# Performance work log

Hardware: AMD Instinct MI355X
Metric: run time of the kernel (lower is better)

The kernel has to match this reference:

```python
import jax, jax.numpy as jnp
import numpy as np

FEATURES = 768

def setup_inputs() -> dict:
    key = jax.random.key(0)
    k1, k2, kq, kd, kc = jax.random.split(key, 5)
    B, S1, S2 = 8, 2048, 2048
    bound = 1.0 / np.sqrt(FEATURES)  # nn.Linear default init range
    return {
        "matrix1": jax.random.normal(k1, (B, S1, FEATURES), dtype=jnp.float32),
        "matrix2": jax.random.normal(k2, (B, S2, FEATURES), dtype=jnp.float32),
        "w_q": jax.random.uniform(kq, (FEATURES,), jnp.float32, -bound, bound),
        "w_d": jax.random.uniform(kd, (FEATURES,), jnp.float32, -bound, bound),
        "w_c": jax.random.uniform(kc, (FEATURES,), jnp.float32, -bound, bound),
    }

def reference(matrix1, matrix2, w_q, w_d, w_c):
    # S[b,j,k] = (m1 @ w_q)[b,j] + (m2 @ w_d)[b,k] + sum_f w_c[f]*m1[b,j,f]*m2[b,k,f]
    Q = jnp.einsum('bjf,f->bj', matrix1, w_q)                # [B, S1]
    D = jnp.einsum('bkf,f->bk', matrix2, w_d)                # [B, S2]
    C = jnp.einsum('bjf,bkf->bjk', matrix1 * w_c, matrix2)   # [B, S1, S2]
    return Q[:, :, None] + D[:, None, :] + C
```

## Files before the change

### kernel.cpp

```cpp
#include <hip/hip_runtime.h>
#include <hip/hip_bf16.h>

#define S1 2048
#define S2 2048
#define FEAT 768
#define NB 8
#define BM 256
#define BN 256
#define BK 32
#define NKT (FEAT / BK)
#define KTILE_BYTES 32768
#define NBUF 4

typedef __attribute__((ext_vector_type(8))) short bf16x8;
typedef __attribute__((ext_vector_type(4))) float f32x4;
typedef __attribute__((ext_vector_type(4))) unsigned short us4;
typedef __attribute__((address_space(1))) const unsigned int gu32;
typedef __attribute__((address_space(3))) unsigned int lu32;

static __device__ __forceinline__ unsigned short f2bf(float x) {
    unsigned u = __builtin_bit_cast(unsigned, x);
    unsigned r = u + 0x7FFFu + ((u >> 16) & 1u);
    return (unsigned short)(r >> 16);
}

__global__ __launch_bounds__(256) void conv_kernel(
    const float* __restrict__ m1, const float* __restrict__ m2,
    const float* __restrict__ wq, const float* __restrict__ wd,
    const float* __restrict__ wc,
    unsigned short* __restrict__ A, unsigned short* __restrict__ Bm,
    float* __restrict__ Q, float* __restrict__ D) {
    int wave = threadIdx.x >> 6;
    int lane = threadIdx.x & 63;
    int g = blockIdx.x * 4 + wave;
    bool isA = (g < NB * S1);
    int row = isA ? g : g - NB * S1;
    const float* src = isA ? m1 : m2;
    const float* w   = isA ? wq : wd;
    unsigned short* dst = (isA ? A : Bm) + (size_t)row * FEAT;
    const float4* rp = (const float4*)(src + (size_t)row * FEAT);
    const float4* wp = (const float4*)w;
    const float4* cp = (const float4*)wc;
    float acc = 0.f;
#pragma unroll
    for (int i = 0; i < 3; ++i) {
        int idx = lane + 64 * i;
        float4 a = rp[idx];
        float4 b = wp[idx];
        acc += a.x * b.x + a.y * b.y + a.z * b.z + a.w * b.w;
        float4 c;
        if (isA) c = cp[idx]; else c = float4{1.f, 1.f, 1.f, 1.f};
        us4 v = { f2bf(a.x * c.x), f2bf(a.y * c.y),
                  f2bf(a.z * c.z), f2bf(a.w * c.w) };
        *(us4*)(dst + idx * 4) = v;
    }
#pragma unroll
    for (int s = 32; s; s >>= 1) acc += __shfl_xor(acc, s, 64);
    if (lane == 0) (isA ? Q : D)[row] = acc;
}

#define STAGE(kt) do {                                                            \
    const int _buf = (kt) & (NBUF - 1);                                           \
    const char* _As = Ab + (kt) * (BK * 2);                                       \
    const char* _Bs = Bb + (kt) * (BK * 2);                                       \
    char* _lA = ldsb + _buf * KTILE_BYTES;                                        \
    char* _lB = _lA + 16384;                                                      \
    _Pragma("unroll")                                                             \
    for (int _r = 0; _r < 2; ++_r) {                                              \
        const int _rowb = _r * 128 + wave * 16;                                   \
        __builtin_amdgcn_global_load_lds(                                         \
            (gu32*)(_As + (size_t)(_rowb + srow) * (FEAT * 2) + scolsw),          \
            (lu32*)(_lA + _rowb * 64), 16, 0, 0);                                 \
        __builtin_amdgcn_global_load_lds(                                         \
            (gu32*)(_Bs + (size_t)(_rowb + srow) * (FEAT * 2) + scolsw),          \
            (lu32*)(_lB + _rowb * 64), 16, 0, 0);                                 \
    }                                                                             \
} while (0)

#define LOADFRAGS(set, ktidx) do {                                                \
    const char* _lA = ldsb + ((ktidx) & (NBUF - 1)) * KTILE_BYTES;                \
    const char* _lB = _lA + 16384;                                                \
    _Pragma("unroll")                                                             \
    for (int _n = 0; _n < 4; ++_n)                                                \
        bfx[set][_n] = *(const bf16x8*)(_lB + (wn * 64 + _n * 16 + fr) * 64 + fkb);\
    _Pragma("unroll")                                                             \
    for (int _m = 0; _m < 8; ++_m)                                                \
        afr[set][_m] = *(const bf16x8*)(_lA + (wm * 128 + _m * 16 + fr) * 64 + fkb);\
} while (0)

__global__ __launch_bounds__(512, 2) void gemm256_kernel(
    const unsigned short* __restrict__ A, const unsigned short* __restrict__ Bm,
    const float* __restrict__ Q, const float* __restrict__ D,
    float* __restrict__ out) {

    extern __shared__ __align__(16) char ldsb[];

    const int bid = blockIdx.x;
    const int swz = (bid & 7) * 64 + (bid >> 3);
    const int b  = swz >> 6;
    const int t  = swz & 63;
    const int tm = t >> 3, tn = t & 7;

    const int tid  = threadIdx.x;
    const int lane = tid & 63;
    const int wave = tid >> 6;
    const int wm = wave >> 2, wn = wave & 3;

    const char* Ab = (const char*)(A + ((size_t)b * S1 + (size_t)tm * BM) * FEAT);
    const char* Bb = (const char*)(Bm + ((size_t)b * S2 + (size_t)tn * BN) * FEAT);

    const int srow   = lane >> 2;
    const int scolsw = (((lane & 3) ^ ((lane >> 3) & 3)) * 16);

    const int fr  = lane & 15;
    const int fkb = (((lane >> 4) ^ ((lane >> 1) & 3)) * 16);

    f32x4 acc[8][4];
#pragma unroll
    for (int m = 0; m < 8; ++m)
#pragma unroll
        for (int n = 0; n < 4; ++n) acc[m][n] = (f32x4)0.f;

    bf16x8 afr[2][8];
    bf16x8 bfx[2][4];

    STAGE(0);
    STAGE(1);
    STAGE(2);
    asm volatile("s_waitcnt vmcnt(4)" ::: "memory");
    __builtin_amdgcn_s_barrier();
    asm volatile("" ::: "memory");
    LOADFRAGS(0, 0);

#pragma unroll 2
    for (int kt = 0; kt < NKT; ++kt) {
        const int cur = kt & 1, nxt = cur ^ 1;
        if (kt + 3 < NKT) STAGE(kt + 3);
        if (kt + 1 < NKT) LOADFRAGS(nxt, kt + 1);

        __builtin_amdgcn_s_setprio(1);
#pragma unroll
        for (int m = 0; m < 8; ++m)
#pragma unroll
            for (int n = 0; n < 4; ++n)
                acc[m][n] = __builtin_amdgcn_mfma_f32_16x16x32_bf16(
                    afr[cur][m], bfx[cur][n], acc[m][n], 0, 0, 0);
        __builtin_amdgcn_s_setprio(0);

        if (kt + 1 < NKT) {
            if (kt + 3 < NKT) asm volatile("s_waitcnt vmcnt(4)" ::: "memory");
            else              asm volatile("s_waitcnt vmcnt(0)" ::: "memory");
            __builtin_amdgcn_s_barrier();
            asm volatile("" ::: "memory");
        }
    }

    const float* Qb = Q + b * S1 + tm * BM;
    const float* Db = D + b * S2 + tn * BN;
    float dv[4];
#pragma unroll
    for (int n = 0; n < 4; ++n) dv[n] = Db[wn * 64 + n * 16 + fr];

    const size_t outbase = ((size_t)b * S1 + (size_t)tm * BM) * S2 + (size_t)tn * BN;
#pragma unroll
    for (int m = 0; m < 8; ++m) {
#pragma unroll
        for (int i = 0; i < 4; ++i) {
            int rl = wm * 128 + m * 16 + (lane >> 4) * 4 + i;
            float qv = Qb[rl];
            float* orow = out + outbase + (size_t)rl * S2 + wn * 64;
#pragma unroll
            for (int n = 0; n < 4; ++n)
                orow[n * 16 + fr] = acc[m][n][i] + qv + dv[n];
        }
    }
}

__global__ __launch_bounds__(256) void qd_kernel(
    const float* __restrict__ m1, const float* __restrict__ m2,
    const float* __restrict__ wq, const float* __restrict__ wd,
    float* __restrict__ Q, float* __restrict__ D) {
    int wave = threadIdx.x >> 6;
    int lane = threadIdx.x & 63;
    int g = blockIdx.x * 4 + wave;
    const float* src; const float* w; float* dst; int row;
    if (g < NB * S1) { src = m1; w = wq; dst = Q; row = g; }
    else             { src = m2; w = wd; dst = D; row = g - NB * S1; }
    const float4* rp = (const float4*)(src + (size_t)row * FEAT);
    const float4* wp = (const float4*)w;
    float acc = 0.f;
#pragma unroll
    for (int i = 0; i < 3; ++i) {
        float4 a = rp[lane + 64 * i];
        float4 b = wp[lane + 64 * i];
        acc += a.x * b.x + a.y * b.y + a.z * b.z + a.w * b.w;
    }
#pragma unroll
    for (int s = 32; s; s >>= 1) acc += __shfl_xor(acc, s, 64);
    if (lane == 0) dst[row] = acc;
}

__global__ __launch_bounds__(256) void gemm_kernel(
    const float* __restrict__ m1, const float* __restrict__ m2,
    const float* __restrict__ wc,
    const float* __restrict__ Q, const float* __restrict__ D,
    float* __restrict__ out) {

    __shared__ __align__(16) char sA[128 * 64 * 2];
    __shared__ __align__(16) char sB[128 * 64 * 2];
    __shared__ float wcs[FEAT];

    const int tid = threadIdx.x;
    const int blk = blockIdx.x;
    const int b  = blk >> 8;
    const int t  = blk & 255;
    const int tm = t >> 4, tn = t & 15;

    for (int i = tid; i < FEAT; i += 256) wcs[i] = wc[i];

    const float* Abase = m1 + ((size_t)b * S1 + (size_t)tm * 128) * FEAT;
    const float* Bbase = m2 + ((size_t)b * S2 + (size_t)tn * 128) * FEAT;

    const int lane = tid & 63;
    const int wave = tid >> 6;
    const int wm = wave >> 1, wn = wave & 1;

    f32x4 acc[4][4];
#pragma unroll
    for (int m = 0; m < 4; ++m)
#pragma unroll
        for (int n = 0; n < 4; ++n) acc[m][n] = (f32x4)0.f;

    const int col4 = tid & 15;
    const int row0 = tid >> 4;

    __syncthreads();

    for (int ks = 0; ks < FEAT / 64; ++ks) {
        float4 wc4 = *(const float4*)&wcs[ks * 64 + col4 * 4];
        const float4* Ak = (const float4*)(Abase + ks * 64);
        const float4* Bk = (const float4*)(Bbase + ks * 64);

        __syncthreads();
#pragma unroll
        for (int i = 0; i < 8; ++i) {
            int r = row0 + 16 * i;
            float4 a = Ak[(size_t)r * (FEAT / 4) + col4];
            us4 av = { f2bf(a.x * wc4.x), f2bf(a.y * wc4.y),
                       f2bf(a.z * wc4.z), f2bf(a.w * wc4.w) };
            int off = r * 128 + ((col4 * 8) ^ ((r & 7) << 4));
            *(us4*)(sA + off) = av;
        }
#pragma unroll
        for (int i = 0; i < 8; ++i) {
            int r = row0 + 16 * i;
            float4 v = Bk[(size_t)r * (FEAT / 4) + col4];
            us4 bv = { f2bf(v.x), f2bf(v.y), f2bf(v.z), f2bf(v.w) };
            int off = r * 128 + ((col4 * 8) ^ ((r & 7) << 4));
            *(us4*)(sB + off) = bv;
        }
        __syncthreads();

#pragma unroll
        for (int s = 0; s < 2; ++s) {
            bf16x8 af[4], bfr[4];
#pragma unroll
            for (int m = 0; m < 4; ++m) {
                int r = wm * 64 + m * 16 + (lane & 15);
                int coff = (s * 64 + (lane >> 4) * 16) ^ ((r & 7) << 4);
                af[m] = *(const bf16x8*)(sA + r * 128 + coff);
            }
#pragma unroll
            for (int n = 0; n < 4; ++n) {
                int r = wn * 64 + n * 16 + (lane & 15);
                int coff = (s * 64 + (lane >> 4) * 16) ^ ((r & 7) << 4);
                bfr[n] = *(const bf16x8*)(sB + r * 128 + coff);
            }
#pragma unroll
            for (int m = 0; m < 4; ++m)
#pragma unroll
                for (int n = 0; n < 4; ++n)
                    acc[m][n] = __builtin_amdgcn_mfma_f32_16x16x32_bf16(
                        af[m], bfr[n], acc[m][n], 0, 0, 0);
        }
    }

    const float* Qb = Q + b * S1 + tm * 128;
    const float* Db = D + b * S2 + tn * 128;
    float dv[4];
#pragma unroll
    for (int n = 0; n < 4; ++n) dv[n] = Db[wn * 64 + n * 16 + (lane & 15)];

    const size_t outbase = ((size_t)b * S1 + (size_t)tm * 128) * S2 + (size_t)tn * 128;
#pragma unroll
    for (int m = 0; m < 4; ++m) {
#pragma unroll
        for (int i = 0; i < 4; ++i) {
            int rl = wm * 64 + m * 16 + (lane >> 4) * 4 + i;
            float qv = Qb[rl];
            float* orow = out + outbase + (size_t)rl * S2 + wn * 64;
#pragma unroll
            for (int n = 0; n < 4; ++n) {
                int cl = n * 16 + (lane & 15);
                orow[cl] = acc[m][n][i] + qv + dv[n];
            }
        }
    }
}

extern "C" void kernel_launch(void* const* d_in, const int* in_sizes, int n_in,
                              void* d_out, int out_size, void* d_ws, size_t ws_size,
                              hipStream_t stream) {
    const float* m1 = (const float*)d_in[0];
    const float* m2 = (const float*)d_in[1];
    const float* wq = (const float*)d_in[2];
    const float* wd = (const float*)d_in[3];
    const float* wc = (const float*)d_in[4];
    float* out = (float*)d_out;

    const size_t elems = (size_t)NB * S1 * FEAT;
    const size_t need = 2 * elems * sizeof(unsigned short)
                      + (size_t)(NB * S1 + NB * S2) * sizeof(float);

    if (ws_size >= need) {
        unsigned short* Abuf = (unsigned short*)d_ws;
        unsigned short* Bbuf = Abuf + elems;
        float* Q  = (float*)(Bbuf + elems);
        float* Dv = Q + NB * S1;
        conv_kernel<<<(NB * S1 + NB * S2) / 4, 256, 0, stream>>>(
            m1, m2, wq, wd, wc, Abuf, Bbuf, Q, Dv);
        gemm256_kernel<<<NB * (S1 / BM) * (S2 / BN), 512, NBUF * KTILE_BYTES, stream>>>(
            Abuf, Bbuf, Q, Dv, out);
    } else {
        float* Q  = (float*)d_ws;
        float* Dv = Q + NB * S1;
        qd_kernel<<<(2 * NB * S1) / 4, 256, 0, stream>>>(m1, m2, wq, wd, Q, Dv);
        gemm_kernel<<<NB * 256, 256, 0, stream>>>(m1, m2, wc, Q, Dv, out);
    }
}
```

Before: 93.29 us.

## Split GEMM main loop into two interleaved phases with staged loads and fragment reads

Each k-iteration now runs as two halves. The A and B global-to-LDS loads and the next-fragment LDS reads are spread across two MFMA clusters, with extra barriers between them, to interleave memory traffic with compute more finely (ping-pong style). Launch bounds drop from 2 to 1 blocks per SM, which gives the compiler more registers but may reduce occupancy. The extra barriers add sync cost per iteration.

```diff
diff --git a/kernel.cpp b/kernel.cpp
--- a/kernel.cpp
+++ b/kernel.cpp
@@ -59,36 +59,17 @@
     if (lane == 0) (isA ? Q : D)[row] = acc;
 }
 
-#define STAGE(kt) do {                                                            \
-    const int _buf = (kt) & (NBUF - 1);                                           \
-    const char* _As = Ab + (kt) * (BK * 2);                                       \
-    const char* _Bs = Bb + (kt) * (BK * 2);                                       \
-    char* _lA = ldsb + _buf * KTILE_BYTES;                                        \
-    char* _lB = _lA + 16384;                                                      \
+#define STAGE_HALF(_src, _ldst) do {                                              \
     _Pragma("unroll")                                                             \
     for (int _r = 0; _r < 2; ++_r) {                                              \
         const int _rowb = _r * 128 + wave * 16;                                   \
         __builtin_amdgcn_global_load_lds(                                         \
-            (gu32*)(_As + (size_t)(_rowb + srow) * (FEAT * 2) + scolsw),          \
-            (lu32*)(_lA + _rowb * 64), 16, 0, 0);                                 \
-        __builtin_amdgcn_global_load_lds(                                         \
-            (gu32*)(_Bs + (size_t)(_rowb + srow) * (FEAT * 2) + scolsw),          \
-            (lu32*)(_lB + _rowb * 64), 16, 0, 0);                                 \
+            (gu32*)((_src) + (size_t)(_rowb + srow) * (FEAT * 2) + scolsw),       \
+            (lu32*)((_ldst) + _rowb * 64), 16, 0, 0);                             \
     }                                                                             \
 } while (0)
 
-#define LOADFRAGS(set, ktidx) do {                                                \
-    const char* _lA = ldsb + ((ktidx) & (NBUF - 1)) * KTILE_BYTES;                \
-    const char* _lB = _lA + 16384;                                                \
-    _Pragma("unroll")                                                             \
-    for (int _n = 0; _n < 4; ++_n)                                                \
-        bfx[set][_n] = *(const bf16x8*)(_lB + (wn * 64 + _n * 16 + fr) * 64 + fkb);\
-    _Pragma("unroll")                                                             \
-    for (int _m = 0; _m < 8; ++_m)                                                \
-        afr[set][_m] = *(const bf16x8*)(_lA + (wm * 128 + _m * 16 + fr) * 64 + fkb);\
-} while (0)
-
-__global__ __launch_bounds__(512, 2) void gemm256_kernel(
+__global__ __launch_bounds__(512, 1) void gemm256_kernel(
     const unsigned short* __restrict__ A, const unsigned short* __restrict__ Bm,
     const float* __restrict__ Q, const float* __restrict__ D,
     float* __restrict__ out) {
@@ -124,32 +105,74 @@
     bf16x8 afr[2][8];
     bf16x8 bfx[2][4];
 
-    STAGE(0);
-    STAGE(1);
-    STAGE(2);
+#pragma unroll
+    for (int pk = 0; pk < 3; ++pk) {
+        char* lA = ldsb + pk * KTILE_BYTES;
+        STAGE_HALF(Ab + pk * (BK * 2), lA);
+        STAGE_HALF(Bb + pk * (BK * 2), lA + 16384);
+    }
     asm volatile("s_waitcnt vmcnt(4)" ::: "memory");
     __builtin_amdgcn_s_barrier();
     asm volatile("" ::: "memory");
-    LOADFRAGS(0, 0);
+    {
+        const char* lA = ldsb;
+        const char* lB = ldsb + 16384;
+#pragma unroll
+        for (int n = 0; n < 4; ++n)
+            bfx[0][n] = *(const bf16x8*)(lB + (wn * 64 + n * 16 + fr) * 64 + fkb);
+#pragma unroll
+        for (int m = 0; m < 8; ++m)
+            afr[0][m] = *(const bf16x8*)(lA + (wm * 128 + m * 16 + fr) * 64 + fkb);
+    }
 
 #pragma unroll 2
     for (int kt = 0; kt < NKT; ++kt) {
         const int cur = kt & 1, nxt = cur ^ 1;
-        if (kt + 3 < NKT) STAGE(kt + 3);
-        if (kt + 1 < NKT) LOADFRAGS(nxt, kt + 1);
-
+        const int lk = kt + 3;
+        const char* nA = ldsb + ((kt + 1) & 3) * KTILE_BYTES;
+        const char* nB = nA + 16384;
+        char* stA = ldsb + (lk & 3) * KTILE_BYTES;
+
+        if (lk < NKT) STAGE_HALF(Ab + lk * (BK * 2), stA);
+        if (kt + 1 < NKT) {
+#pragma unroll
+            for (int n = 0; n < 4; ++n)
+                bfx[nxt][n] = *(const bf16x8*)(nB + (wn * 64 + n * 16 + fr) * 64 + fkb);
+#pragma unroll
+            for (int m = 0; m < 2; ++m)
+                afr[nxt][m] = *(const bf16x8*)(nA + (wm * 128 + m * 16 + fr) * 64 + fkb);
+        }
+        __builtin_amdgcn_s_barrier();
+        asm volatile("" ::: "memory");
         __builtin_amdgcn_s_setprio(1);
 #pragma unroll
-        for (int m = 0; m < 8; ++m)
+        for (int m = 0; m < 4; ++m)
 #pragma unroll
             for (int n = 0; n < 4; ++n)
                 acc[m][n] = __builtin_amdgcn_mfma_f32_16x16x32_bf16(
                     afr[cur][m], bfx[cur][n], acc[m][n], 0, 0, 0);
         __builtin_amdgcn_s_setprio(0);
 
+        if (lk < NKT) STAGE_HALF(Bb + lk * (BK * 2), stA + 16384);
         if (kt + 1 < NKT) {
-            if (kt + 3 < NKT) asm volatile("s_waitcnt vmcnt(4)" ::: "memory");
-            else              asm volatile("s_waitcnt vmcnt(0)" ::: "memory");
+#pragma unroll
+            for (int m = 2; m < 8; ++m)
+                afr[nxt][m] = *(const bf16x8*)(nA + (wm * 128 + m * 16 + fr) * 64 + fkb);
+        }
+        __builtin_amdgcn_s_barrier();
+        asm volatile("" ::: "memory");
+        __builtin_amdgcn_s_setprio(1);
+#pragma unroll
+        for (int m = 4; m < 8; ++m)
+#pragma unroll
+            for (int n = 0; n < 4; ++n)
+                acc[m][n] = __builtin_amdgcn_mfma_f32_16x16x32_bf16(
+                    afr[cur][m], bfx[cur][n], acc[m][n], 0, 0, 0);
+        __builtin_amdgcn_s_setprio(0);
+
+        if (kt + 1 < NKT) {
+            if (lk < NKT) asm volatile("s_waitcnt vmcnt(4)" ::: "memory");
+            else          asm volatile("s_waitcnt vmcnt(0)" ::: "memory");
             __builtin_amdgcn_s_barrier();
             asm volatile("" ::: "memory");
         }
```

Measured after the change: 93.27 us. Within noise of the previous version (-0.0%).
